# Optimization experiments

Measured on AMD Instinct MI355X. Metric: run time of the kernel, lower is better.

Reference implementation:

```python
import jax, jax.numpy as jnp
import numpy as np

B, N, DPOS, F, P, K = 32, 1024, 3, 64, 128, 16


def setup_inputs() -> dict:
    key = jax.random.key(0)
    kp, kf, kw1, kw2 = jax.random.split(key, 4)
    points = jax.random.normal(kp, (B, N, DPOS), dtype=jnp.float32)
    features = jax.random.normal(kf, (B, N, F), dtype=jnp.float32)
    W1 = jax.random.normal(kw1, (2 * F, 2 * P), dtype=jnp.float32) * (1.0 / np.sqrt(2 * F))
    b1 = jnp.zeros((2 * P,), dtype=jnp.float32)
    W2 = jax.random.normal(kw2, (2 * P, P), dtype=jnp.float32) * (1.0 / np.sqrt(2 * P))
    b2 = jnp.zeros((P,), dtype=jnp.float32)
    return {"points": points, "features": features, "W1": W1, "b1": b1, "W2": W2, "b2": b2}


def reference(points, features, W1, b1, W2, b2):
    # pairwise squared distances: r_i - 2 p_i.p_j + r_j + 1e-5  -> [B, N, N]
    r = jnp.sum(points * points, axis=2, keepdims=True)
    m = jnp.einsum('bnd,bmd->bnm', points, points)
    D = r - 2.0 * m + jnp.swapaxes(r, 1, 2) + 1e-5
    # K+1 nearest (incl. self), drop self -> indices [B, N, K]
    _, idx = jax.lax.top_k(-D, K + 1)
    idx = idx[:, :, 1:]
    # gather neighbor features: [B, N, K, F]
    neighbors = features[jnp.arange(B)[:, None, None], idx]
    center = jnp.broadcast_to(features[:, :, None, :], neighbors.shape)
    local = jnp.concatenate([neighbors - center, center], axis=-1)  # [B,N,K,2F]
    # 2-layer MLP with exact GELU
    h = jax.nn.gelu(jnp.einsum('bnkf,fh->bnkh', local, W1) + b1, approximate=False)
    out = jax.nn.gelu(jnp.einsum('bnkh,hp->bnkp', h, W2) + b2, approximate=False)
    # mean over neighbors -> [B, N, P]
    return jnp.mean(out, axis=2)
```

## Files before the change

kernel.cpp:

```cpp
#include <hip/hip_runtime.h>
#include <math.h>

#define BB 32
#define NN 1024
#define FF 64
#define PP 128
#define KNN 16
#define H2 256
#define F2 128
#define KSEL 17
#define SVCAP 272

typedef float f32x4 __attribute__((ext_vector_type(4)));
typedef __bf16 bf16x8 __attribute__((ext_vector_type(8)));

__device__ __forceinline__ float gelu_fast(float x) {
    float u = x * (1.0f + 0.044715f * x * x);
    float e = __builtin_amdgcn_exp2f(-2.3022115f * u);
    return x * __builtin_amdgcn_rcpf(1.0f + e);
}

__global__ __launch_bounds__(512, 8) void knn_select(const float* __restrict__ points,
                                                     int* __restrict__ idx_out) {
    __shared__ float4 pts[NN];
    __shared__ unsigned sv_val[8][SVCAP];
    __shared__ unsigned sv_idx[8][SVCAP];
    __shared__ unsigned tie_idx[8][64];

    const int t = threadIdx.x;
    const int w = t >> 6, lane = t & 63;
    const int b = blockIdx.x >> 7;
    const int q0 = (blockIdx.x & 127) * 8;
    const float* pb = points + (size_t)b * NN * 3;
    const unsigned long long lt = (1ull << lane) - 1ull;

    for (int i = t; i < NN; i += 512) {
        float x = pb[3 * i], y = pb[3 * i + 1], z = pb[3 * i + 2];
        float r = __fadd_rn(__fadd_rn(__fmul_rn(x, x), __fmul_rn(y, y)), __fmul_rn(z, z));
        pts[i] = make_float4(x, y, z, r);
    }
    __syncthreads();

    const int qn = q0 + w;
    const int gq = b * NN + qn;
    const float4 qp = pts[qn];

    float D[16];
#pragma unroll
    for (int j = 0; j < 16; ++j) {
        float4 c = pts[j * 64 + lane];
        float dot = __fadd_rn(__fadd_rn(__fmul_rn(qp.x, c.x), __fmul_rn(qp.y, c.y)),
                              __fmul_rn(qp.z, c.z));
        D[j] = __fadd_rn(__fadd_rn(__fsub_rn(qp.w, __fmul_rn(2.0f, dot)), c.w), 1e-5f);
    }

    float mnf = D[0];
#pragma unroll
    for (int j = 1; j < 16; ++j) mnf = fminf(mnf, D[j]);
    const unsigned mbits = __float_as_uint(mnf);

    unsigned T = 0;
#pragma unroll
    for (int bit = 31; bit >= 0; --bit) {
        unsigned cand = T | (1u << bit);
        int cnt = __popcll(__ballot(mbits < cand));
        if (cnt < KSEL) T = cand;
    }

    unsigned base = 0;
#pragma unroll
    for (int j = 0; j < 16; ++j) {
        unsigned vb = __float_as_uint(D[j]);
        bool keep = (vb <= T);
        unsigned long long m = __ballot(keep);
        if (keep) {
            unsigned pos = base + (unsigned)__popcll(m & lt);
            if (pos < SVCAP) { sv_val[w][pos] = vb; sv_idx[w][pos] = j * 64 + lane; }
        }
        base += (unsigned)__popcll(m);
    }
    unsigned C = base > SVCAP ? SVCAP : base;
    const int S = (int)((C + 63) >> 6);

    unsigned Ts = 0;
    if (S == 1) {
        unsigned xv0 = (lane < (int)C) ? sv_val[w][lane] : 0xFFFFFFFFu;
#pragma unroll
        for (int bit = 31; bit >= 0; --bit) {
            unsigned cand = Ts | (1u << bit);
            int cnt = __popcll(__ballot(xv0 < cand));
            if (cnt < KSEL) Ts = cand;
        }
    } else {
        for (int bit = 31; bit >= 0; --bit) {
            unsigned cand = Ts | (1u << bit);
            int cnt = 0;
            for (int s = 0; s < S; ++s) {
                int i = s * 64 + lane;
                unsigned vb = (i < (int)C) ? sv_val[w][i] : 0xFFFFFFFFu;
                cnt += __popcll(__ballot(vb < cand));
            }
            if (cnt < KSEL) Ts = cand;
        }
    }

    int L = 0;
    for (int s = 0; s < S; ++s) {
        int i = s * 64 + lane;
        unsigned vb = (i < (int)C) ? sv_val[w][i] : 0xFFFFFFFFu;
        L += __popcll(__ballot(vb < Ts));
    }
    const int need = KSEL - L;

    unsigned vmin_l = 0xFFFFFFFFu;
    for (int s = 0; s < S; ++s) {
        int i = s * 64 + lane;
        unsigned vb = (i < (int)C) ? sv_val[w][i] : 0xFFFFFFFFu;
        vmin_l = vmin_l < vb ? vmin_l : vb;
    }
#pragma unroll
    for (int off = 32; off >= 1; off >>= 1) {
        unsigned o2 = __shfl_xor(vmin_l, off, 64);
        vmin_l = vmin_l < o2 ? vmin_l : o2;
    }
    const unsigned Vmin = vmin_l;
    unsigned imin_l = 0xFFFFFFFFu;
    for (int s = 0; s < S; ++s) {
        int i = s * 64 + lane;
        unsigned vb = (i < (int)C) ? sv_val[w][i] : 0xFFFFFFFFu;
        unsigned mi = (i < (int)C) ? sv_idx[w][i] : 0xFFFFFFFFu;
        if (vb == Vmin && mi < imin_l) imin_l = mi;
    }
#pragma unroll
    for (int off = 32; off >= 1; off >>= 1) {
        unsigned o2 = __shfl_xor(imin_l, off, 64);
        imin_l = imin_l < o2 ? imin_l : o2;
    }
    const unsigned dropIdx = imin_l;

    int* o = idx_out + (size_t)gq * KNN;
    unsigned wbase = 0, tbase = 0;
    for (int s = 0; s < S; ++s) {
        int i = s * 64 + lane;
        unsigned vb = (i < (int)C) ? sv_val[w][i] : 0xFFFFFFFFu;
        unsigned mi = (i < (int)C) ? sv_idx[w][i] : 0xFFFFFFFFu;
        bool wk = (vb < Ts) && (mi != dropIdx);
        unsigned long long wm = __ballot(wk);
        if (wk) o[wbase + (unsigned)__popcll(wm & lt)] = (int)mi;
        wbase += (unsigned)__popcll(wm);
        bool tk = (vb == Ts);
        unsigned long long tm2 = __ballot(tk);
        if (tk) {
            unsigned tp = tbase + (unsigned)__popcll(tm2 & lt);
            if (tp < 64) tie_idx[w][tp] = mi;
        }
        tbase += (unsigned)__popcll(tm2);
    }
    unsigned tc = tbase > 64 ? 64 : tbase;
    if ((int)tc == need) {
        bool tk = (lane < (int)tc);
        unsigned mi2 = tk ? tie_idx[w][lane] : 0xFFFFFFFFu;
        tk = tk && (mi2 != dropIdx);
        unsigned long long m3 = __ballot(tk);
        if (tk) o[wbase + (unsigned)__popcll(m3 & lt)] = (int)mi2;
    } else if (lane == 0) {
        unsigned pos = wbase;
        for (int r = 0; r < need; ++r) {
            unsigned best = 0xFFFFFFFFu; int bj = 0;
            for (int j2 = 0; j2 < (int)tc; ++j2) {
                unsigned mi = tie_idx[w][j2];
                if (mi < best) { best = mi; bj = j2; }
            }
            tie_idx[w][bj] = 0xFFFFFFFFu;
            if (best != dropIdx) o[pos++] = (int)best;
        }
    }
}

__global__ __launch_bounds__(256) void prep_frag(const float* __restrict__ W1,
                                                 const float* __restrict__ W2,
                                                 __bf16* __restrict__ Wcf,
                                                 __bf16* __restrict__ W2f) {
    int tid = blockIdx.x * 256 + threadIdx.x;
    if (tid < 4096) {
        const int lane = tid & 63, quad = lane >> 4, l16 = lane & 15;
        const int kk = (tid >> 6) & 1, n_tile = tid >> 7;
        const int n = n_tile * 16 + l16;
        const int kb = kk * 32 + quad * 8;
        bf16x8 v;
#pragma unroll
        for (int j = 0; j < 8; ++j) {
            const int k = kb + j;
            float x = (n < 256) ? W1[k * 256 + n]
                                : (W1[(64 + k) * 256 + (n - 256)] - W1[k * 256 + (n - 256)]);
            v[j] = (__bf16)x;
        }
        *(bf16x8*)(Wcf + (size_t)tid * 8) = v;
    } else {
        const int t2 = tid - 4096;
        const int lane = t2 & 63, quad = lane >> 4, l16 = lane & 15;
        const int nt = (t2 >> 6) & 7, kk8 = t2 >> 9;
        const int p = nt * 16 + l16;
        const int hb = kk8 * 32 + quad * 8;
        bf16x8 v;
#pragma unroll
        for (int j = 0; j < 8; ++j) v[j] = (__bf16)W2[(size_t)(hb + j) * PP + p];
        *(bf16x8*)(W2f + (size_t)t2 * 8) = v;
    }
}

__global__ __launch_bounds__(256, 4) void gq_gemm(const float* __restrict__ feat,
                                                  const __bf16* __restrict__ Wcf,
                                                  const float* __restrict__ b1,
                                                  __bf16* __restrict__ Gall,
                                                  __bf16* __restrict__ Qall) {
    __shared__ __align__(16) __bf16 st[4][16][136];
    const int t = threadIdx.x, w = t >> 6, lane = t & 63;
    const int quad = lane >> 4, l16 = lane & 15;
    const int m0 = blockIdx.x * 16;

    bf16x8 a[2];
#pragma unroll
    for (int kk = 0; kk < 2; ++kk) {
        const float* ap = feat + (size_t)(m0 + l16) * 64 + kk * 32 + quad * 8;
        float4 a0 = *(const float4*)ap, a1 = *(const float4*)(ap + 4);
        bf16x8 v;
        v[0] = (__bf16)a0.x; v[1] = (__bf16)a0.y; v[2] = (__bf16)a0.z; v[3] = (__bf16)a0.w;
        v[4] = (__bf16)a1.x; v[5] = (__bf16)a1.y; v[6] = (__bf16)a1.z; v[7] = (__bf16)a1.w;
        a[kk] = v;
    }
    f32x4 acc[8];
#pragma unroll
    for (int nt = 0; nt < 8; ++nt) acc[nt] = (f32x4){0.f, 0.f, 0.f, 0.f};
#pragma unroll
    for (int kk = 0; kk < 2; ++kk)
#pragma unroll
        for (int nt = 0; nt < 8; ++nt) {
            bf16x8 bf = *(const bf16x8*)(Wcf + (size_t)(((w * 8 + nt) * 2 + kk) * 64 + lane) * 8);
            acc[nt] = __builtin_amdgcn_mfma_f32_16x16x32_bf16(a[kk], bf, acc[nt], 0, 0, 0);
        }

    const bool isQ = (w >= 2);
#pragma unroll
    for (int nt = 0; nt < 8; ++nt) {
        const int col = nt * 16 + l16;
        const float bias = isQ ? b1[(w - 2) * 128 + col] : 0.f;
#pragma unroll
        for (int r = 0; r < 4; ++r)
            st[w][quad * 4 + r][col] = (__bf16)(acc[nt][r] + bias);
    }
    __syncthreads();

    const int row = lane >> 2, c = lane & 3;
    const int m = m0 + row;
#pragma unroll
    for (int i = 0; i < 4; ++i) {
        const int col = c * 32 + i * 8;
        bf16x8 v = *(const bf16x8*)&st[w][row][col];
        if (!isQ) *(bf16x8*)(Gall + (size_t)m * H2 + w * 128 + col) = v;
        else      *(bf16x8*)(Qall + (size_t)m * H2 + (w - 2) * 128 + col) = v;
    }
}

__global__ __launch_bounds__(512, 4) void fused_mlp3(const __bf16* __restrict__ Gall,
                                                     const __bf16* __restrict__ Qall,
                                                     const int* __restrict__ knn_idx,
                                                     const __bf16* __restrict__ W2f,
                                                     const float* __restrict__ b2,
                                                     float* __restrict__ out) {
    __shared__ __align__(16) __bf16 w2s[32768];
    const int t = threadIdx.x, w = t >> 6, lane = t & 63;
    const int quad = lane >> 4, l16 = lane & 15;

#pragma unroll
    for (int i = 0; i < 8; ++i) {
        bf16x8 v = *(const bf16x8*)(W2f + (size_t)(i * 512 + t) * 8);
        *(bf16x8*)&w2s[(size_t)(i * 512 + t) * 8] = v;
    }
    __syncthreads();

    const int wave_id = blockIdx.x * 8 + w;

    float bias[8];
#pragma unroll
    for (int nt = 0; nt < 8; ++nt) bias[nt] = b2[nt * 16 + l16];

#pragma unroll
    for (int it = 0; it < 2; ++it) {
        const int q0 = wave_id * 4 + it * 2;
        const int b = q0 >> 10;
        const int nb0 = knn_idx[q0 * KNN + l16];
        const int nb1 = knn_idx[(q0 + 1) * KNN + l16];
        const __bf16* g0 = Gall + ((size_t)(b << 10) + nb0) * H2;
        const __bf16* g1 = Gall + ((size_t)(b << 10) + nb1) * H2;
        const __bf16* qq0 = Qall + (size_t)q0 * H2;
        const __bf16* qq1 = qq0 + H2;

        f32x4 acc[2][8];
#pragma unroll
        for (int tm = 0; tm < 2; ++tm)
#pragma unroll
            for (int nt = 0; nt < 8; ++nt) acc[tm][nt] = (f32x4){0.f, 0.f, 0.f, 0.f};

#pragma unroll
        for (int kk8 = 0; kk8 < 8; ++kk8) {
            const int ho = kk8 * 32 + quad * 8;
            bf16x8 gA = *(const bf16x8*)(g0 + ho);
            bf16x8 qA = *(const bf16x8*)(qq0 + ho);
            bf16x8 gB = *(const bf16x8*)(g1 + ho);
            bf16x8 qB = *(const bf16x8*)(qq1 + ho);
            bf16x8 a0, a1;
#pragma unroll
            for (int j = 0; j < 8; ++j) {
                a0[j] = (__bf16)gelu_fast((float)gA[j] + (float)qA[j]);
                a1[j] = (__bf16)gelu_fast((float)gB[j] + (float)qB[j]);
            }
            const __bf16* bb = &w2s[kk8 * 8 * 512 + lane * 8];
#pragma unroll
            for (int nt = 0; nt < 8; ++nt) {
                bf16x8 bf = *(const bf16x8*)(bb + nt * 512);
                acc[0][nt] = __builtin_amdgcn_mfma_f32_16x16x32_bf16(a0, bf, acc[0][nt], 0, 0, 0);
                acc[1][nt] = __builtin_amdgcn_mfma_f32_16x16x32_bf16(a1, bf, acc[1][nt], 0, 0, 0);
            }
        }

#pragma unroll
        for (int tm = 0; tm < 2; ++tm)
#pragma unroll
            for (int nt = 0; nt < 8; ++nt) {
                float s = 0.f;
#pragma unroll
                for (int r = 0; r < 4; ++r) s += gelu_fast(acc[tm][nt][r] + bias[nt]);
                s += __shfl_xor(s, 16, 64);
                s += __shfl_xor(s, 32, 64);
                if (quad == 0)
                    out[(size_t)(q0 + tm) * PP + nt * 16 + l16] = s * 0.0625f;
            }
    }
}

extern "C" void kernel_launch(void* const* d_in, const int* in_sizes, int n_in,
                              void* d_out, int out_size, void* d_ws, size_t ws_size,
                              hipStream_t stream) {
    const float* points   = (const float*)d_in[0];
    const float* features = (const float*)d_in[1];
    const float* W1 = (const float*)d_in[2];
    const float* b1 = (const float*)d_in[3];
    const float* W2 = (const float*)d_in[4];
    const float* b2 = (const float*)d_in[5];
    float* out = (float*)d_out;

    const size_t IDX_B  = (size_t)BB * NN * KNN * 4;
    const size_t WCF_B  = 512 * 64 * 2;
    const size_t W2F_B  = 256 * 128 * 2;
    const size_t G_B    = (size_t)BB * NN * H2 * 2;

    int* knn_idx = (int*)d_ws;
    char* p = (char*)d_ws + IDX_B;
    __bf16* Wcf  = (__bf16*)p;  p += WCF_B;
    __bf16* W2f  = (__bf16*)p;  p += W2F_B;
    __bf16* Gall = (__bf16*)p;  p += G_B;
    __bf16* Qall = (__bf16*)p;

    prep_frag<<<32, 256, 0, stream>>>(W1, W2, Wcf, W2f);
    knn_select<<<BB * 128, 512, 0, stream>>>(points, knn_idx);
    gq_gemm<<<2048, 256, 0, stream>>>(features, Wcf, b1, Gall, Qall);
    fused_mlp3<<<1024, 512, 0, stream>>>(Gall, Qall, knn_idx, W2f, b2, out);
}
```

Measured before the change: 213.9 us.

## Drop LDS W2 staging, one query per wave, remap blocks for XCD locality

The final MLP kernel no longer stages W2 in shared memory. Each wave now reads W2 fragments directly from global memory (through the cache) and handles a single query instead of four, and the grid grows fourfold with a higher occupancy hint. Block indices are swizzled so consecutive logical blocks land across the 8 XCDs, aiming at better L2 locality for the Gall gathers. The GELU polynomial is also refolded into one fma. The trade is fewer registers, no LDS and higher occupancy against repeated global/L2 reads of W2 per wave and less reuse of each B fragment.

```diff
diff --git a/kernel.cpp b/kernel.cpp
--- a/kernel.cpp
+++ b/kernel.cpp
@@ -15,8 +15,9 @@
 typedef __bf16 bf16x8 __attribute__((ext_vector_type(8)));
 
 __device__ __forceinline__ float gelu_fast(float x) {
-    float u = x * (1.0f + 0.044715f * x * x);
-    float e = __builtin_amdgcn_exp2f(-2.3022115f * u);
+    float s = x * x;
+    float arg = x * fmaf(s, -0.1029438f, -2.3022115f);
+    float e = __builtin_amdgcn_exp2f(arg);
     return x * __builtin_amdgcn_rcpf(1.0f + e);
 }
 
@@ -262,80 +263,56 @@
     }
 }
 
-__global__ __launch_bounds__(512, 4) void fused_mlp3(const __bf16* __restrict__ Gall,
+__global__ __launch_bounds__(512, 6) void fused_mlp5(const __bf16* __restrict__ Gall,
                                                      const __bf16* __restrict__ Qall,
                                                      const int* __restrict__ knn_idx,
                                                      const __bf16* __restrict__ W2f,
                                                      const float* __restrict__ b2,
                                                      float* __restrict__ out) {
-    __shared__ __align__(16) __bf16 w2s[32768];
     const int t = threadIdx.x, w = t >> 6, lane = t & 63;
     const int quad = lane >> 4, l16 = lane & 15;
 
-#pragma unroll
-    for (int i = 0; i < 8; ++i) {
-        bf16x8 v = *(const bf16x8*)(W2f + (size_t)(i * 512 + t) * 8);
-        *(bf16x8*)&w2s[(size_t)(i * 512 + t) * 8] = v;
-    }
-    __syncthreads();
-
-    const int wave_id = blockIdx.x * 8 + w;
-
-    float bias[8];
-#pragma unroll
-    for (int nt = 0; nt < 8; ++nt) bias[nt] = b2[nt * 16 + l16];
-
-#pragma unroll
-    for (int it = 0; it < 2; ++it) {
-        const int q0 = wave_id * 4 + it * 2;
-        const int b = q0 >> 10;
-        const int nb0 = knn_idx[q0 * KNN + l16];
-        const int nb1 = knn_idx[(q0 + 1) * KNN + l16];
-        const __bf16* g0 = Gall + ((size_t)(b << 10) + nb0) * H2;
-        const __bf16* g1 = Gall + ((size_t)(b << 10) + nb1) * H2;
-        const __bf16* qq0 = Qall + (size_t)q0 * H2;
-        const __bf16* qq1 = qq0 + H2;
-
-        f32x4 acc[2][8];
-#pragma unroll
-        for (int tm = 0; tm < 2; ++tm)
-#pragma unroll
-            for (int nt = 0; nt < 8; ++nt) acc[tm][nt] = (f32x4){0.f, 0.f, 0.f, 0.f};
-
-#pragma unroll
-        for (int kk8 = 0; kk8 < 8; ++kk8) {
-            const int ho = kk8 * 32 + quad * 8;
-            bf16x8 gA = *(const bf16x8*)(g0 + ho);
-            bf16x8 qA = *(const bf16x8*)(qq0 + ho);
-            bf16x8 gB = *(const bf16x8*)(g1 + ho);
-            bf16x8 qB = *(const bf16x8*)(qq1 + ho);
-            bf16x8 a0, a1;
-#pragma unroll
-            for (int j = 0; j < 8; ++j) {
-                a0[j] = (__bf16)gelu_fast((float)gA[j] + (float)qA[j]);
-                a1[j] = (__bf16)gelu_fast((float)gB[j] + (float)qB[j]);
-            }
-            const __bf16* bb = &w2s[kk8 * 8 * 512 + lane * 8];
-#pragma unroll
-            for (int nt = 0; nt < 8; ++nt) {
-                bf16x8 bf = *(const bf16x8*)(bb + nt * 512);
-                acc[0][nt] = __builtin_amdgcn_mfma_f32_16x16x32_bf16(a0, bf, acc[0][nt], 0, 0, 0);
-                acc[1][nt] = __builtin_amdgcn_mfma_f32_16x16x32_bf16(a1, bf, acc[1][nt], 0, 0, 0);
-            }
-        }
-
-#pragma unroll
-        for (int tm = 0; tm < 2; ++tm)
-#pragma unroll
-            for (int nt = 0; nt < 8; ++nt) {
-                float s = 0.f;
-#pragma unroll
-                for (int r = 0; r < 4; ++r) s += gelu_fast(acc[tm][nt][r] + bias[nt]);
-                s += __shfl_xor(s, 16, 64);
-                s += __shfl_xor(s, 32, 64);
-                if (quad == 0)
-                    out[(size_t)(q0 + tm) * PP + nt * 16 + l16] = s * 0.0625f;
-            }
+    const int phys = blockIdx.x;
+    const int blk = ((phys & 7) << 9) | (phys >> 3);
+
+    const int q = blk * 8 + w;
+    const int b = q >> 10;
+
+    const int nb = knn_idx[q * KNN + l16];
+    const __bf16* g0 = Gall + ((size_t)(b << 10) + nb) * H2;
+    const __bf16* qq = Qall + (size_t)q * H2;
+
+    f32x4 acc[8];
+#pragma unroll
+    for (int nt = 0; nt < 8; ++nt) acc[nt] = (f32x4){0.f, 0.f, 0.f, 0.f};
+
+#pragma unroll
+    for (int kk8 = 0; kk8 < 8; ++kk8) {
+        const int ho = kk8 * 32 + quad * 8;
+        bf16x8 gA = *(const bf16x8*)(g0 + ho);
+        bf16x8 qA = *(const bf16x8*)(qq + ho);
+        bf16x8 a0;
+#pragma unroll
+        for (int j = 0; j < 8; ++j)
+            a0[j] = (__bf16)gelu_fast((float)gA[j] + (float)qA[j]);
+        const __bf16* bb = W2f + ((size_t)(kk8 * 8) * 64 + lane) * 8;
+#pragma unroll
+        for (int nt = 0; nt < 8; ++nt) {
+            bf16x8 bf = *(const bf16x8*)(bb + (size_t)nt * 512);
+            acc[nt] = __builtin_amdgcn_mfma_f32_16x16x32_bf16(a0, bf, acc[nt], 0, 0, 0);
+        }
+    }
+
+#pragma unroll
+    for (int nt = 0; nt < 8; ++nt) {
+        const float bias = b2[nt * 16 + l16];
+        float s = 0.f;
+#pragma unroll
+        for (int r = 0; r < 4; ++r) s += gelu_fast(acc[nt][r] + bias);
+        s += __shfl_xor(s, 16, 64);
+        s += __shfl_xor(s, 32, 64);
+        if (quad == 0)
+            out[(size_t)q * PP + nt * 16 + l16] = s * 0.0625f;
     }
 }
 
@@ -365,5 +342,5 @@
     prep_frag<<<32, 256, 0, stream>>>(W1, W2, Wcf, W2f);
     knn_select<<<BB * 128, 512, 0, stream>>>(points, knn_idx);
     gq_gemm<<<2048, 256, 0, stream>>>(features, Wcf, b1, Gall, Qall);
-    fused_mlp3<<<1024, 512, 0, stream>>>(Gall, Qall, knn_idx, W2f, b2, out);
-}
+    fused_mlp5<<<4096, 512, 0, stream>>>(Gall, Qall, knn_idx, W2f, b2, out);
+}
```

Measured after the change: 244.4 us. 1.14x slower.

## Merge weight prep into kNN launch and halve MLP shared memory for occupancy

Applied to the files above, without the earlier changes.

The weight-fragment preparation now runs as extra blocks of the kNN selection kernel, saving one kernel launch. The fused MLP kernel stages W2 in two halves through a 32KB shared buffer instead of 64KB. It processes two queries per wave instead of four and launches twice as many blocks with a higher occupancy bound, to improve latency hiding on the gathered loads. GELU's polynomial is folded into one FMA. In exchange, W2 is loaded into shared memory once per block for fewer queries, and each block adds an extra barrier.

```diff
diff --git a/kernel.cpp b/kernel.cpp
--- a/kernel.cpp
+++ b/kernel.cpp
@@ -15,13 +15,48 @@
 typedef __bf16 bf16x8 __attribute__((ext_vector_type(8)));
 
 __device__ __forceinline__ float gelu_fast(float x) {
-    float u = x * (1.0f + 0.044715f * x * x);
-    float e = __builtin_amdgcn_exp2f(-2.3022115f * u);
+    float s = x * x;
+    float arg = x * fmaf(s, -0.1029438f, -2.3022115f);
+    float e = __builtin_amdgcn_exp2f(arg);
     return x * __builtin_amdgcn_rcpf(1.0f + e);
 }
 
-__global__ __launch_bounds__(512, 8) void knn_select(const float* __restrict__ points,
-                                                     int* __restrict__ idx_out) {
+__global__ __launch_bounds__(512, 8) void knn_prep(const float* __restrict__ points,
+                                                   int* __restrict__ idx_out,
+                                                   const float* __restrict__ W1,
+                                                   const float* __restrict__ W2,
+                                                   __bf16* __restrict__ Wcf,
+                                                   __bf16* __restrict__ W2f) {
+    if (blockIdx.x >= 4096) {
+        int tid = (blockIdx.x - 4096) * 512 + threadIdx.x;
+        if (tid < 4096) {
+            const int lane = tid & 63, quad = lane >> 4, l16 = lane & 15;
+            const int kk = (tid >> 6) & 1, n_tile = tid >> 7;
+            const int n = n_tile * 16 + l16;
+            const int kb = kk * 32 + quad * 8;
+            bf16x8 v;
+#pragma unroll
+            for (int j = 0; j < 8; ++j) {
+                const int k = kb + j;
+                float x = (n < 256) ? W1[k * 256 + n]
+                                    : (W1[(64 + k) * 256 + (n - 256)] - W1[k * 256 + (n - 256)]);
+                v[j] = (__bf16)x;
+            }
+            *(bf16x8*)(Wcf + (size_t)tid * 8) = v;
+        } else {
+            const int t2 = tid - 4096;
+            const int lane = t2 & 63, quad = lane >> 4, l16 = lane & 15;
+            const int nt = (t2 >> 6) & 7, kk8 = t2 >> 9;
+            const int p = nt * 16 + l16;
+            const int hb = kk8 * 32 + quad * 8;
+            bf16x8 v;
+#pragma unroll
+            for (int j = 0; j < 8; ++j) v[j] = (__bf16)W2[(size_t)(hb + j) * PP + p];
+            *(bf16x8*)(W2f + (size_t)t2 * 8) = v;
+        }
+        return;
+    }
+
     __shared__ float4 pts[NN];
     __shared__ unsigned sv_val[8][SVCAP];
     __shared__ unsigned sv_idx[8][SVCAP];
@@ -177,38 +212,6 @@
     }
 }
 
-__global__ __launch_bounds__(256) void prep_frag(const float* __restrict__ W1,
-                                                 const float* __restrict__ W2,
-                                                 __bf16* __restrict__ Wcf,
-                                                 __bf16* __restrict__ W2f) {
-    int tid = blockIdx.x * 256 + threadIdx.x;
-    if (tid < 4096) {
-        const int lane = tid & 63, quad = lane >> 4, l16 = lane & 15;
-        const int kk = (tid >> 6) & 1, n_tile = tid >> 7;
-        const int n = n_tile * 16 + l16;
-        const int kb = kk * 32 + quad * 8;
-        bf16x8 v;
-#pragma unroll
-        for (int j = 0; j < 8; ++j) {
-            const int k = kb + j;
-            float x = (n < 256) ? W1[k * 256 + n]
-                                : (W1[(64 + k) * 256 + (n - 256)] - W1[k * 256 + (n - 256)]);
-            v[j] = (__bf16)x;
-        }
-        *(bf16x8*)(Wcf + (size_t)tid * 8) = v;
-    } else {
-        const int t2 = tid - 4096;
-        const int lane = t2 & 63, quad = lane >> 4, l16 = lane & 15;
-        const int nt = (t2 >> 6) & 7, kk8 = t2 >> 9;
-        const int p = nt * 16 + l16;
-        const int hb = kk8 * 32 + quad * 8;
-        bf16x8 v;
-#pragma unroll
-        for (int j = 0; j < 8; ++j) v[j] = (__bf16)W2[(size_t)(hb + j) * PP + p];
-        *(bf16x8*)(W2f + (size_t)t2 * 8) = v;
-    }
-}
-
 __global__ __launch_bounds__(256, 4) void gq_gemm(const float* __restrict__ feat,
                                                   const __bf16* __restrict__ Wcf,
                                                   const float* __restrict__ b1,
@@ -262,49 +265,45 @@
     }
 }
 
-__global__ __launch_bounds__(512, 4) void fused_mlp3(const __bf16* __restrict__ Gall,
+__global__ __launch_bounds__(512, 8) void fused_mlp6(const __bf16* __restrict__ Gall,
                                                      const __bf16* __restrict__ Qall,
                                                      const int* __restrict__ knn_idx,
                                                      const __bf16* __restrict__ W2f,
                                                      const float* __restrict__ b2,
                                                      float* __restrict__ out) {
-    __shared__ __align__(16) __bf16 w2s[32768];
+    __shared__ __align__(16) __bf16 w2s[16384];
     const int t = threadIdx.x, w = t >> 6, lane = t & 63;
     const int quad = lane >> 4, l16 = lane & 15;
 
-#pragma unroll
-    for (int i = 0; i < 8; ++i) {
-        bf16x8 v = *(const bf16x8*)(W2f + (size_t)(i * 512 + t) * 8);
-        *(bf16x8*)&w2s[(size_t)(i * 512 + t) * 8] = v;
-    }
-    __syncthreads();
-
     const int wave_id = blockIdx.x * 8 + w;
-
-    float bias[8];
-#pragma unroll
-    for (int nt = 0; nt < 8; ++nt) bias[nt] = b2[nt * 16 + l16];
-
-#pragma unroll
-    for (int it = 0; it < 2; ++it) {
-        const int q0 = wave_id * 4 + it * 2;
-        const int b = q0 >> 10;
-        const int nb0 = knn_idx[q0 * KNN + l16];
-        const int nb1 = knn_idx[(q0 + 1) * KNN + l16];
-        const __bf16* g0 = Gall + ((size_t)(b << 10) + nb0) * H2;
-        const __bf16* g1 = Gall + ((size_t)(b << 10) + nb1) * H2;
-        const __bf16* qq0 = Qall + (size_t)q0 * H2;
-        const __bf16* qq1 = qq0 + H2;
-
-        f32x4 acc[2][8];
-#pragma unroll
-        for (int tm = 0; tm < 2; ++tm)
-#pragma unroll
-            for (int nt = 0; nt < 8; ++nt) acc[tm][nt] = (f32x4){0.f, 0.f, 0.f, 0.f};
-
-#pragma unroll
-        for (int kk8 = 0; kk8 < 8; ++kk8) {
-            const int ho = kk8 * 32 + quad * 8;
+    const int q0 = wave_id * 2;
+    const int b = q0 >> 10;
+    const int nb0 = knn_idx[q0 * KNN + l16];
+    const int nb1 = knn_idx[(q0 + 1) * KNN + l16];
+    const __bf16* g0 = Gall + ((size_t)(b << 10) + nb0) * H2;
+    const __bf16* g1 = Gall + ((size_t)(b << 10) + nb1) * H2;
+    const __bf16* qq0 = Qall + (size_t)q0 * H2;
+    const __bf16* qq1 = qq0 + H2;
+
+    f32x4 acc[2][8];
+#pragma unroll
+    for (int tm = 0; tm < 2; ++tm)
+#pragma unroll
+        for (int nt = 0; nt < 8; ++nt) acc[tm][nt] = (f32x4){0.f, 0.f, 0.f, 0.f};
+
+#pragma unroll
+    for (int half = 0; half < 2; ++half) {
+        if (half) __syncthreads();
+#pragma unroll
+        for (int i = 0; i < 4; ++i) {
+            bf16x8 v = *(const bf16x8*)(W2f + (size_t)(half * 2048 + i * 512 + t) * 8);
+            *(bf16x8*)&w2s[(size_t)(i * 512 + t) * 8] = v;
+        }
+        __syncthreads();
+
+#pragma unroll
+        for (int kl = 0; kl < 4; ++kl) {
+            const int ho = (half * 4 + kl) * 32 + quad * 8;
             bf16x8 gA = *(const bf16x8*)(g0 + ho);
             bf16x8 qA = *(const bf16x8*)(qq0 + ho);
             bf16x8 gB = *(const bf16x8*)(g1 + ho);
@@ -315,7 +314,7 @@
                 a0[j] = (__bf16)gelu_fast((float)gA[j] + (float)qA[j]);
                 a1[j] = (__bf16)gelu_fast((float)gB[j] + (float)qB[j]);
             }
-            const __bf16* bb = &w2s[kk8 * 8 * 512 + lane * 8];
+            const __bf16* bb = &w2s[(kl * 8) * 512 + lane * 8];
 #pragma unroll
             for (int nt = 0; nt < 8; ++nt) {
                 bf16x8 bf = *(const bf16x8*)(bb + nt * 512);
@@ -323,20 +322,21 @@
                 acc[1][nt] = __builtin_amdgcn_mfma_f32_16x16x32_bf16(a1, bf, acc[1][nt], 0, 0, 0);
             }
         }
-
-#pragma unroll
-        for (int tm = 0; tm < 2; ++tm)
-#pragma unroll
-            for (int nt = 0; nt < 8; ++nt) {
-                float s = 0.f;
-#pragma unroll
-                for (int r = 0; r < 4; ++r) s += gelu_fast(acc[tm][nt][r] + bias[nt]);
-                s += __shfl_xor(s, 16, 64);
-                s += __shfl_xor(s, 32, 64);
-                if (quad == 0)
-                    out[(size_t)(q0 + tm) * PP + nt * 16 + l16] = s * 0.0625f;
-            }
-    }
+    }
+
+#pragma unroll
+    for (int tm = 0; tm < 2; ++tm)
+#pragma unroll
+        for (int nt = 0; nt < 8; ++nt) {
+            const float bias = b2[nt * 16 + l16];
+            float s = 0.f;
+#pragma unroll
+            for (int r = 0; r < 4; ++r) s += gelu_fast(acc[tm][nt][r] + bias);
+            s += __shfl_xor(s, 16, 64);
+            s += __shfl_xor(s, 32, 64);
+            if (quad == 0)
+                out[(size_t)(q0 + tm) * PP + nt * 16 + l16] = s * 0.0625f;
+        }
 }
 
 extern "C" void kernel_launch(void* const* d_in, const int* in_sizes, int n_in,
@@ -362,8 +362,7 @@
     __bf16* Gall = (__bf16*)p;  p += G_B;
     __bf16* Qall = (__bf16*)p;
 
-    prep_frag<<<32, 256, 0, stream>>>(W1, W2, Wcf, W2f);
-    knn_select<<<BB * 128, 512, 0, stream>>>(points, knn_idx);
+    knn_prep<<<4112, 512, 0, stream>>>(points, knn_idx, W1, W2, Wcf, W2f);
     gq_gemm<<<2048, 256, 0, stream>>>(features, Wcf, b1, Gall, Qall);
-    fused_mlp3<<<1024, 512, 0, stream>>>(Gall, Qall, knn_idx, W2f, b2, out);
-}
+    fused_mlp6<<<2048, 512, 0, stream>>>(Gall, Qall, knn_idx, W2f, b2, out);
+}
```

Result: slower. 478.0 us (+123.5%).
